# Performance work log

Hardware: AMD Instinct MI355X
Metric: run time of the kernel (lower is better)

The kernel has to match this reference:

```python
import jax, jax.numpy as jnp
import numpy as np


def lstm_cell(x, h, c, Wi, Wh, b):
    # PyTorch LSTMCell gate order: i, f, g, o
    g = x @ Wi.T + h @ Wh.T + b
    i, f, gg, o = jnp.split(g, 4, axis=-1)
    c = jax.nn.sigmoid(f) * c + jax.nn.sigmoid(i) * jnp.tanh(gg)
    h = jax.nn.sigmoid(o) * jnp.tanh(c)
    return h, c


def setup_inputs() -> dict:
    key = jax.random.key(0)
    ks = jax.random.split(key, 32)
    S, B, L, N, T = 20, 16, 30, 6, 20
    H, E, Vs, Vt = 512, 512, 50000, 30000
    w = lambda k, shape: jax.random.normal(k, shape, jnp.float32) * 0.05
    return {
        'articles': jax.random.randint(ks[0], (S, B, L), 0, Vs, jnp.int32),
        'summaries': jax.random.randint(ks[1], (N, B, T), 0, Vt, jnp.int32),
        'emb_src': w(ks[2], (Vs, E)),
        'emb_tgt': w(ks[3], (Vt, E)),
        'we_Wi': w(ks[4], (4 * H, E)), 'we_Wh': w(ks[5], (4 * H, H)), 'we_b': w(ks[6], (4 * H,)),
        'se_Wi': w(ks[7], (4 * H, H)), 'se_Wh': w(ks[8], (4 * H, H)), 'se_b': w(ks[9], (4 * H,)),
        'W_feat': w(ks[10], (H, H)), 'b_feat': w(ks[11], (H,)),
        'wd_Wi': w(ks[12], (4 * H, E)), 'wd_Wh': w(ks[13], (4 * H, H)), 'wd_b': w(ks[14], (4 * H,)),
        'W_vocab': w(ks[15], (Vt, H)), 'b_vocab': w(ks[16], (Vt,)),
        'sd_Wi': w(ks[17], (4 * H, H)), 'sd_Wh': w(ks[18], (4 * H, H)), 'sd_b': w(ks[19], (4 * H,)),
        'attn_Wh': w(ks[20], (H, H)), 'attn_wc': w(ks[21], (H,)), 'attn_v': w(ks[22], (H,)),
        'W_out': w(ks[23], (H, 2 * H)), 'b_out': w(ks[24], (H,)),
    }


def _forward(articles, summaries, emb_src, emb_tgt, we_Wi, we_Wh, we_b,
             se_Wi, se_Wh, se_b, W_feat, b_feat, wd_Wi, wd_Wh, wd_b,
             W_vocab, b_vocab, sd_Wi, sd_Wh, sd_b, attn_Wh, attn_wc, attn_v,
             W_out, b_out):
    S, B, L = articles.shape
    H = we_Wh.shape[1]

    # ---- word encoder: LSTMCell over each sentence, vmapped over S ----
    def encode_sentence(tokens):  # [B, L]
        x = emb_src[tokens]  # [B, L, E]
        z = jnp.zeros((B, H), x.dtype)
        def step(hc, xt):
            h, c = lstm_cell(xt, hc[0], hc[1], we_Wi, we_Wh, we_b)
            return (h, c), None
        (h, _), _ = jax.lax.scan(step, (z, z), jnp.swapaxes(x, 0, 1))
        return h
    word_hx = jax.vmap(encode_sentence)(articles)  # [S, B, H]

    # ---- sentence encoder: LSTM over sentence dim ----
    z = jnp.zeros((B, H), word_hx.dtype)
    def senc_step(hc, x):
        h, c = lstm_cell(x, hc[0], hc[1], se_Wi, se_Wh, se_b)
        return (h, c), h
    (s_hx, s_cx), sent_out = jax.lax.scan(senc_step, (z, z), word_hx)  # sent_out [S,B,H]
    sent_feat = sent_out @ W_feat.T + b_feat  # precomputed attention features

    mask = (articles[:, :, 0:1] > 0).astype(jnp.float32)  # [S, B, 1]
    coverage0 = jnp.zeros_like(mask)

    # ---- hierarchical decoder over summary sentences ----
    def sent_step(carry, sent):  # sent [B, T]
        w_hx, w_cx, s_hx, s_cx, coverage, loss = carry
        seq = sent.T  # [T, B]

        def word_step(wc, ba):
            wh, wcell, l = wc
            wb, wa = ba
            wh, wcell = lstm_cell(emb_tgt[wb], wh, wcell, wd_Wi, wd_Wh, wd_b)
            logits = wh @ W_vocab.T + b_vocab  # [B, V]
            logp = jax.nn.log_softmax(logits, axis=-1)
            nll = -jnp.take_along_axis(logp, wa[:, None], axis=1)[:, 0]
            m = (wa != 0).astype(logits.dtype)  # ignore_index=0
            l = l + jnp.sum(nll * m) / jnp.maximum(jnp.sum(m), 1.0)
            return (wh, wcell, l), None

        (w_hx, w_cx, loss), _ = jax.lax.scan(word_step, (w_hx, w_cx, loss), (seq[:-1], seq[1:]))

        # sentence decoder step with coverage attention over S sentences
        s_h2, s_cx = lstm_cell(w_hx, s_hx, s_cx, sd_Wi, sd_Wh, sd_b)
        e = jnp.einsum('sbh,h->sb', jnp.tanh(sent_feat + s_h2 @ attn_Wh.T + coverage * attn_wc), attn_v)
        e = jnp.where(mask[:, :, 0] > 0, e, -1e9)
        align = jax.nn.softmax(e, axis=0)[:, :, None]  # [S, B, 1]
        context = jnp.sum(align * sent_out, axis=0)  # [B, H]
        final = jnp.tanh(jnp.concatenate([context, s_h2], axis=-1) @ W_out.T + b_out)
        # coverage loss (with pre-update coverage), then accumulate coverage
        loss = loss + jnp.mean(jnp.sum(jnp.minimum(align[:, :, 0], coverage[:, :, 0]), axis=0))
        coverage = coverage + align
        return (final, w_cx, final, s_cx, coverage, loss), None

    init = (s_hx, s_cx, s_hx, s_cx, coverage0, jnp.float32(0.0))
    (_, _, _, _, _, loss), _ = jax.lax.scan(sent_step, init, summaries)
    return loss


def reference(articles, summaries, emb_src, emb_tgt, we_Wi, we_Wh, we_b,
              se_Wi, se_Wh, se_b, W_feat, b_feat, wd_Wi, wd_Wh, wd_b,
              W_vocab, b_vocab, sd_Wi, sd_Wh, sd_b, attn_Wh, attn_wc, attn_v,
              W_out, b_out):
    return _forward(articles, summaries, emb_src, emb_tgt, we_Wi, we_Wh, we_b,
                    se_Wi, se_Wh, se_b, W_feat, b_feat, wd_Wi, wd_Wh, wd_b,
                    W_vocab, b_vocab, sd_Wi, sd_Wh, sd_b, attn_Wh, attn_wc,
                    attn_v, W_out, b_out)
```

## Files before the change

### kernel.cpp

```cpp
#include <hip/hip_runtime.h>
#include <cstdint>
#include <cstddef>

#define H 512
#define SS 20
#define BB 16
#define LL 30
#define NN 6
#define TT 20
#define VT 30000
#define MROWS 1824
#define NSTEPS 114
#define MPAD 1856
#define NT2 120
#define VBLK 232
#define UBLK 16

typedef __attribute__((ext_vector_type(8))) short bf16x8;
typedef __attribute__((ext_vector_type(4))) float f32x4;

__device__ __forceinline__ float sigmoidf_(float x) { return 1.f / (1.f + expf(-x)); }
__device__ __forceinline__ float b2f(ushort u) { return __uint_as_float(((uint32_t)u) << 16); }
__device__ __forceinline__ ushort f2b_rne(float f) {
  uint32_t u = __float_as_uint(f);
  return (ushort)((u + 0x7fffu + ((u >> 16) & 1u)) >> 16);
}

__device__ __forceinline__ void gbar(uint* cnt, uint* gen, uint nblk)
{
  __syncthreads();
  if (threadIdx.x == 0) {
    uint g = __hip_atomic_load(gen, __ATOMIC_RELAXED, __HIP_MEMORY_SCOPE_AGENT);
    uint v = __hip_atomic_fetch_add(cnt, 1u, __ATOMIC_ACQ_REL, __HIP_MEMORY_SCOPE_AGENT);
    if (v == nblk - 1u) {
      __hip_atomic_store(cnt, 0u, __ATOMIC_RELAXED, __HIP_MEMORY_SCOPE_AGENT);
      __hip_atomic_store(gen, g + 1u, __ATOMIC_RELEASE, __HIP_MEMORY_SCOPE_AGENT);
    } else {
      while (__hip_atomic_load(gen, __ATOMIC_ACQUIRE, __HIP_MEMORY_SCOPE_AGENT) == g)
        __builtin_amdgcn_s_sleep(2);
    }
  }
  __syncthreads();
}

struct PrepP {
  const int* articles; const int* summaries;
  const float* emb_src; const float* emb_tgt;
  const float* we_Wi; const float* wd_Wi; const float* we_Wh;
  const float* se_Wi; const float* se_Wh; const float* W_feat;
  const float* wd_Wh; const float* sd_Wi; const float* sd_Wh;
  const float* attn_Wh; const float* W_out;
  ushort* A_we; ushort* A_wd;
  ushort* weWi; ushort* wdWi; ushort* weWh;
  ushort* seWi; ushort* seWh; ushort* wfeat;
  ushort* wdWh; ushort* sdWi; ushort* sdWh;
  ushort* attnWh; ushort* Wout;
};

__device__ __forceinline__ void conv_f2b(const float* __restrict__ src,
                                         ushort* __restrict__ dst, int n4,
                                         int t0, int stride)
{
  for (int i = t0; i < n4; i += stride) {
    float4 v = reinterpret_cast<const float4*>(src)[i];
    ushort4 o;
    o.x = f2b_rne(v.x); o.y = f2b_rne(v.y);
    o.z = f2b_rne(v.z); o.w = f2b_rne(v.w);
    reinterpret_cast<ushort4*>(dst)[i] = o;
  }
}

__global__ __launch_bounds__(256) void prep_kernel(PrepP P)
{
  const int t0 = blockIdx.x * 256 + threadIdx.x;
  const int stride = gridDim.x * 256;
  for (int i = t0; i < SS * BB * LL * H; i += stride) {
    int m = i >> 9, k = i & 511;
    int l = m / (SS * BB), sb = m % (SS * BB);
    int tok = P.articles[sb * LL + l];
    P.A_we[i] = f2b_rne(P.emb_src[(size_t)tok * H + k]);
  }
  for (int i = t0; i < MROWS * H; i += stride) {
    int m = i >> 9, k = i & 511;
    int stp = m >> 4, b = m & 15;
    int n = stp / (TT - 1), t = stp % (TT - 1);
    int tok = P.summaries[(n * BB + b) * TT + t];
    P.A_wd[i] = f2b_rne(P.emb_tgt[(size_t)tok * H + k]);
  }
  const int Q = 4 * H * H / 4;
  conv_f2b(P.we_Wi, P.weWi, Q, t0, stride);
  conv_f2b(P.wd_Wi, P.wdWi, Q, t0, stride);
  conv_f2b(P.we_Wh, P.weWh, Q, t0, stride);
  conv_f2b(P.se_Wi, P.seWi, Q, t0, stride);
  conv_f2b(P.se_Wh, P.seWh, Q, t0, stride);
  conv_f2b(P.wd_Wh, P.wdWh, Q, t0, stride);
  conv_f2b(P.sd_Wi, P.sdWi, Q, t0, stride);
  conv_f2b(P.sd_Wh, P.sdWh, Q, t0, stride);
  conv_f2b(P.W_feat, P.wfeat, H * H / 4, t0, stride);
  conv_f2b(P.attn_Wh, P.attnWh, H * H / 4, t0, stride);
  conv_f2b(P.W_out, P.Wout, H * 2 * H / 4, t0, stride);
}

__global__ __launch_bounds__(512) void proj_mfma_kernel(
    const ushort* __restrict__ A_we, const ushort* __restrict__ weWi,
    const float* __restrict__ we_b, ushort* __restrict__ XiW,
    const ushort* __restrict__ A_wd, const ushort* __restrict__ wdWi,
    const float* __restrict__ wd_b, ushort* __restrict__ XiD)
{
  int bid = blockIdx.x;
  const ushort* A; const ushort* W; const float* bias; ushort* C; int M, mt, nt;
  if (bid < 1200) { A = A_we; W = weWi; bias = we_b; C = XiW; M = 9600; mt = bid >> 3; nt = bid & 7; }
  else { int b2 = bid - 1200; A = A_wd; W = wdWi; bias = wd_b; C = XiD; M = MROWS; mt = b2 >> 3; nt = b2 & 7; }
  const int tid = threadIdx.x, wid = tid >> 6, lane = tid & 63;
  const int wm = wid >> 2, wn = wid & 3;
  const int m0 = mt * 64 + wm * 32, n0 = nt * 256 + wn * 64;
  const int lr = lane & 15, lk = (lane >> 4) << 3;

  f32x4 acc[2][4];
#pragma unroll
  for (int i = 0; i < 2; ++i)
#pragma unroll
    for (int nf = 0; nf < 4; ++nf) acc[i][nf] = (f32x4)0.0f;

  for (int k0 = 0; k0 < H; k0 += 32) {
    bf16x8 a[2], b[4];
#pragma unroll
    for (int i = 0; i < 2; ++i) {
      int m = m0 + i * 16 + lr;
      bf16x8 az = (bf16x8)(short)0;
      if (m < M) az = *reinterpret_cast<const bf16x8*>(A + (size_t)m * H + k0 + lk);
      a[i] = az;
    }
#pragma unroll
    for (int nf = 0; nf < 4; ++nf)
      b[nf] = *reinterpret_cast<const bf16x8*>(W + (size_t)(n0 + nf * 16 + lr) * H + k0 + lk);
#pragma unroll
    for (int i = 0; i < 2; ++i)
#pragma unroll
      for (int nf = 0; nf < 4; ++nf)
        acc[i][nf] = __builtin_amdgcn_mfma_f32_16x16x32_bf16(a[i], b[nf], acc[i][nf], 0, 0, 0);
  }
#pragma unroll
  for (int i = 0; i < 2; ++i)
#pragma unroll
    for (int nf = 0; nf < 4; ++nf) {
      int n = n0 + nf * 16 + lr;
      float bv = bias[n];
#pragma unroll
      for (int jreg = 0; jreg < 4; ++jreg) {
        int row = m0 + i * 16 + (lane >> 4) * 4 + jreg;
        if (row < M) C[(size_t)row * 2048 + n] = f2b_rne(acc[i][nf][jreg] + bv);
      }
    }
}

struct UP {
  const ushort* XiW; const ushort* XiD;
  const ushort* weWh; const ushort* seWi; const ushort* seWh;
  const ushort* wfeat; const ushort* wdWh; const ushort* sdWi;
  const ushort* sdWh; const ushort* attnWh; const ushort* Wout;
  const float* se_b; const float* b_feat; const float* sd_b; const float* b_out;
  const float* attn_wc; const float* attn_v; const int* articles;
  ushort* h0; ushort* h1;
  float* XiS;
  ushort* sh0; ushort* sh1;
  float* sent_out; ushort* sent_out_bf; float* sent_feat;
  ushort* wh_bf; ushort* sdh_bf; ushort* final_bf; ushort* catb;
  float* qb; float* ebuf; float* alignb; float* covb; float* loss;
  uint* bcnt; uint* bgen;
};

__global__ __launch_bounds__(512) void uni_kernel(UP P)
{
  __shared__ f32x4 hred[2][4][64];
  const int tid = threadIdx.x, bid = blockIdx.x;
  const int wid = tid >> 6, lane = tid & 63;
  const int gw = bid * 8 + wid;
  const int lr = lane & 15;
  const int lk = (lane >> 4) << 3;
  const int orow = (lane >> 4) << 2;

  {
    float cst[5][4];
#pragma unroll
    for (int it = 0; it < 5; ++it)
#pragma unroll
      for (int rg = 0; rg < 4; ++rg) cst[it][rg] = 0.f;
    ushort* cur = P.h0;
    ushort* nxt = P.h1;
    const int ug = gw & 31;
    const int unit = ug * 16 + lr;
    const ushort* wb = P.weWh + (size_t)(ug * 16 + lr) * H + lk;
    for (int l = 0; l < LL; ++l) {
#pragma unroll
      for (int it = 0; it < 5; ++it) {
        int item = gw + it * 128;
        int mt = item >> 5;
        f32x4 acc[4];
#pragma unroll
        for (int g = 0; g < 4; ++g) acc[g] = (f32x4)0.0f;
        const ushort* ab = cur + (size_t)(mt * 16 + lr) * H + lk;
#pragma unroll
        for (int k0 = 0; k0 < H; k0 += 32) {
          bf16x8 a = *reinterpret_cast<const bf16x8*>(ab + k0);
#pragma unroll
          for (int g = 0; g < 4; ++g) {
            bf16x8 b = *reinterpret_cast<const bf16x8*>(wb + (size_t)g * H * H + k0);
            acc[g] = __builtin_amdgcn_mfma_f32_16x16x32_bf16(a, b, acc[g], 0, 0, 0);
          }
        }
#pragma unroll
        for (int rg = 0; rg < 4; ++rg) {
          int row = mt * 16 + orow + rg;
          const ushort* xi = P.XiW + (size_t)(l * 320 + row) * 2048 + unit;
          float gi = acc[0][rg] + b2f(xi[0]);
          float gf = acc[1][rg] + b2f(xi[512]);
          float gc = acc[2][rg] + b2f(xi[1024]);
          float go = acc[3][rg] + b2f(xi[1536]);
          float c = sigmoidf_(gf) * cst[it][rg] + sigmoidf_(gi) * tanhf(gc);
          float h = sigmoidf_(go) * tanhf(c);
          cst[it][rg] = c;
          nxt[(size_t)row * H + unit] = f2b_rne(h);
        }
      }
      gbar(P.bcnt, P.bgen, UBLK);
      ushort* t = cur; cur = nxt; nxt = t;
    }
    {
      const ushort* wbs = P.seWi + (size_t)(ug * 16 + lr) * H + lk;
#pragma unroll
      for (int it = 0; it < 5; ++it) {
        int item = gw + it * 128;
        int mt = item >> 5;
        f32x4 acc[4];
#pragma unroll
        for (int g = 0; g < 4; ++g) acc[g] = (f32x4)0.0f;
        const ushort* ab = cur + (size_t)(mt * 16 + lr) * H + lk;
#pragma unroll
        for (int k0 = 0; k0 < H; k0 += 32) {
          bf16x8 a = *reinterpret_cast<const bf16x8*>(ab + k0);
#pragma unroll
          for (int g = 0; g < 4; ++g) {
            bf16x8 b = *reinterpret_cast<const bf16x8*>(wbs + (size_t)g * H * H + k0);
            acc[g] = __builtin_amdgcn_mfma_f32_16x16x32_bf16(a, b, acc[g], 0, 0, 0);
          }
        }
#pragma unroll
        for (int rg = 0; rg < 4; ++rg) {
          int row = mt * 16 + orow + rg;
#pragma unroll
          for (int g = 0; g < 4; ++g)
            P.XiS[(size_t)row * 2048 + g * H + unit] = acc[g][rg] + P.se_b[g * H + unit];
        }
      }
    }
    gbar(P.bcnt, P.bgen, UBLK);
  }

  float cw[4] = {0.f, 0.f, 0.f, 0.f};
  float csd[4] = {0.f, 0.f, 0.f, 0.f};
  {
    float cse[4] = {0.f, 0.f, 0.f, 0.f};
    ushort* cur = P.sh0;
    ushort* nxt = P.sh1;
    const int ug = bid * 2 + wid;
    const int unit = ug * 16 + lr;
    for (int s = 0; s < SS; ++s) {
      if (wid < 2) {
        f32x4 acc[4];
#pragma unroll
        for (int g = 0; g < 4; ++g) acc[g] = (f32x4)0.0f;
        const ushort* ab = cur + (size_t)lr * H + lk;
        const ushort* wb = P.seWh + (size_t)(ug * 16 + lr) * H + lk;
#pragma unroll
        for (int k0 = 0; k0 < H; k0 += 32) {
          bf16x8 a = *reinterpret_cast<const bf16x8*>(ab + k0);
#pragma unroll
          for (int g = 0; g < 4; ++g) {
            bf16x8 b = *reinterpret_cast<const bf16x8*>(wb + (size_t)g * H * H + k0);
            acc[g] = __builtin_amdgcn_mfma_f32_16x16x32_bf16(a, b, acc[g], 0, 0, 0);
          }
        }
#pragma unroll
        for (int rg = 0; rg < 4; ++rg) {
          int row = orow + rg;
          const float* xi = P.XiS + (size_t)(s * 16 + row) * 2048 + unit;
          float gi = acc[0][rg] + xi[0];
          float gf = acc[1][rg] + xi[512];
          float gc = acc[2][rg] + xi[1024];
          float go = acc[3][rg] + xi[1536];
          float c = sigmoidf_(gf) * cse[rg] + sigmoidf_(gi) * tanhf(gc);
          float h = sigmoidf_(go) * tanhf(c);
          cse[rg] = c;
          nxt[(size_t)row * H + unit] = f2b_rne(h);
          P.sent_out[(size_t)(s * 16 + row) * H + unit] = h;
          P.sent_out_bf[(size_t)(s * 16 + row) * H + unit] = f2b_rne(h);
        }
      }
      gbar(P.bcnt, P.bgen, UBLK);
      ushort* t = cur; cur = nxt; nxt = t;
    }
    if (wid < 2) {
      f32x4 v; v[0] = cse[0]; v[1] = cse[1]; v[2] = cse[2]; v[3] = cse[3];
      hred[wid][0][lane] = v;
#pragma unroll
      for (int rg = 0; rg < 4; ++rg) csd[rg] = cse[rg];
    }
    __syncthreads();
    if (wid < 4 && !(wid & 1)) {
      f32x4 v = hred[wid >> 1][0][lane];
      cw[0] = v[0]; cw[1] = v[1]; cw[2] = v[2]; cw[3] = v[3];
    }
    __syncthreads();
  }

  {
    const int ug = gw & 31;
    const int unit = ug * 16 + lr;
    const ushort* wb = P.wfeat + (size_t)(ug * 16 + lr) * H + lk;
#pragma unroll
    for (int it = 0; it < 5; ++it) {
      int item = gw + it * 128;
      int mt = item >> 5;
      f32x4 acc = (f32x4)0.0f;
      const ushort* ab = P.sent_out_bf + (size_t)(mt * 16 + lr) * H + lk;
#pragma unroll
      for (int k0 = 0; k0 < H; k0 += 32) {
        bf16x8 a = *reinterpret_cast<const bf16x8*>(ab + k0);
        bf16x8 b = *reinterpret_cast<const bf16x8*>(wb + k0);
        acc = __builtin_amdgcn_mfma_f32_16x16x32_bf16(a, b, acc, 0, 0, 0);
      }
#pragma unroll
      for (int rg = 0; rg < 4; ++rg) {
        int row = mt * 16 + orow + rg;
        P.sent_feat[(size_t)row * H + unit] = acc[rg] + P.b_feat[unit];
      }
    }
    gbar(P.bcnt, P.bgen, UBLK);
  }

  {
    const int half = wid & 1;
    const int ug2 = bid * 2 + (wid >> 1);
    const int unit2 = ug2 * 16 + lr;
    const int ug = bid * 2 + wid;
    const int unit = ug * 16 + lr;

    for (int n = 0; n < NN; ++n) {
      bf16x8 wreg[4][8];
      if (wid < 4) {
#pragma unroll
        for (int g = 0; g < 4; ++g)
#pragma unroll
          for (int kk = 0; kk < 8; ++kk)
            wreg[g][kk] = *reinterpret_cast<const bf16x8*>(
                P.wdWh + (size_t)g * H * H + (size_t)(ug2 * 16 + lr) * H +
                half * 256 + kk * 32 + lk);
      }
      for (int t = 0; t < TT - 1; ++t) {
        int stp = n * (TT - 1) + t;
        f32x4 acc[4];
        if (wid < 4) {
          const ushort* A = (t == 0)
              ? ((n == 0) ? P.sh0 : P.final_bf)
              : P.wh_bf + (size_t)(stp - 1) * 16 * H;
#pragma unroll
          for (int g = 0; g < 4; ++g) acc[g] = (f32x4)0.0f;
          const ushort* ab = A + (size_t)lr * H + half * 256 + lk;
#pragma unroll
          for (int kk = 0; kk < 8; ++kk) {
            bf16x8 a = *reinterpret_cast<const bf16x8*>(ab + kk * 32);
#pragma unroll
            for (int g = 0; g < 4; ++g)
              acc[g] = __builtin_amdgcn_mfma_f32_16x16x32_bf16(a, wreg[g][kk], acc[g], 0, 0, 0);
          }
          if (half) {
#pragma unroll
            for (int g = 0; g < 4; ++g) hred[wid >> 1][g][lane] = acc[g];
          }
        }
        __syncthreads();
        if (wid < 4 && !half) {
#pragma unroll
          for (int g = 0; g < 4; ++g) {
            f32x4 o = hred[wid >> 1][g][lane];
            acc[g] += o;
          }
#pragma unroll
          for (int rg = 0; rg < 4; ++rg) {
            int row = orow + rg;
            const ushort* xi = P.XiD + (size_t)(stp * 16 + row) * 2048 + unit2;
            float gi = acc[0][rg] + b2f(xi[0]);
            float gf = acc[1][rg] + b2f(xi[512]);
            float gc = acc[2][rg] + b2f(xi[1024]);
            float go = acc[3][rg] + b2f(xi[1536]);
            float c = sigmoidf_(gf) * cw[rg] + sigmoidf_(gi) * tanhf(gc);
            float h = sigmoidf_(go) * tanhf(c);
            cw[rg] = c;
            P.wh_bf[(size_t)(stp * 16 + row) * H + unit2] = f2b_rne(h);
          }
        }
        gbar(P.bcnt, P.bgen, UBLK);
      }
      if (wid < 2) {
        f32x4 acc[4];
#pragma unroll
        for (int g = 0; g < 4; ++g) acc[g] = (f32x4)0.0f;
        const ushort* A1 = P.wh_bf + (size_t)(n * (TT - 1) + TT - 2) * 16 * H;
        const ushort* A2 = (n == 0) ? P.sh0 : P.final_bf;
        const ushort* ab1 = A1 + (size_t)lr * H + lk;
        const ushort* wb1 = P.sdWi + (size_t)(ug * 16 + lr) * H + lk;
#pragma unroll
        for (int k0 = 0; k0 < H; k0 += 32) {
          bf16x8 a = *reinterpret_cast<const bf16x8*>(ab1 + k0);
#pragma unroll
          for (int g = 0; g < 4; ++g) {
            bf16x8 b = *reinterpret_cast<const bf16x8*>(wb1 + (size_t)g * H * H + k0);
            acc[g] = __builtin_amdgcn_mfma_f32_16x16x32_bf16(a, b, acc[g], 0, 0, 0);
          }
        }
        const ushort* ab2 = A2 + (size_t)lr * H + lk;
        const ushort* wb2 = P.sdWh + (size_t)(ug * 16 + lr) * H + lk;
#pragma unroll
        for (int k0 = 0; k0 < H; k0 += 32) {
          bf16x8 a = *reinterpret_cast<const bf16x8*>(ab2 + k0);
#pragma unroll
          for (int g = 0; g < 4; ++g) {
            bf16x8 b = *reinterpret_cast<const bf16x8*>(wb2 + (size_t)g * H * H + k0);
            acc[g] = __builtin_amdgcn_mfma_f32_16x16x32_bf16(a, b, acc[g], 0, 0, 0);
          }
        }
#pragma unroll
        for (int rg = 0; rg < 4; ++rg) {
          int row = orow + rg;
          float gi = acc[0][rg] + P.sd_b[0 * H + unit];
          float gf = acc[1][rg] + P.sd_b[1 * H + unit];
          float gc = acc[2][rg] + P.sd_b[2 * H + unit];
          float go = acc[3][rg] + P.sd_b[3 * H + unit];
          float c = sigmoidf_(gf) * csd[rg] + sigmoidf_(gi) * tanhf(gc);
          float h = sigmoidf_(go) * tanhf(c);
          csd[rg] = c;
          P.sdh_bf[(size_t)row * H + unit] = f2b_rne(h);
        }
      }
      gbar(P.bcnt, P.bgen, UBLK);
      if (wid < 2) {
        f32x4 acc = (f32x4)0.0f;
        const ushort* ab = P.sdh_bf + (size_t)lr * H + lk;
        const ushort* wb = P.attnWh + (size_t)(ug * 16 + lr) * H + lk;
#pragma unroll
        for (int k0 = 0; k0 < H; k0 += 32) {
          bf16x8 a = *reinterpret_cast<const bf16x8*>(ab + k0);
          bf16x8 b = *reinterpret_cast<const bf16x8*>(wb + k0);
          acc = __builtin_amdgcn_mfma_f32_16x16x32_bf16(a, b, acc, 0, 0, 0);
        }
#pragma unroll
        for (int rg = 0; rg < 4; ++rg)
          P.qb[(size_t)(orow + rg) * H + unit] = acc[rg];
      }
      gbar(P.bcnt, P.bgen, UBLK);
      for (int sb = gw; sb < 320; sb += 128) {
        int b = sb & 15;
        float cov = P.covb[sb];
        float sum = 0.f;
        for (int h2 = lane; h2 < H; h2 += 64)
          sum += tanhf(P.sent_feat[(size_t)sb * H + h2] + P.qb[b * H + h2] +
                       cov * P.attn_wc[h2]) * P.attn_v[h2];
#pragma unroll
        for (int d = 1; d < 64; d <<= 1) sum += __shfl_xor(sum, d);
        if (lane == 0)
          P.ebuf[sb] = (P.articles[sb * LL] > 0) ? sum : -1e9f;
      }
      gbar(P.bcnt, P.bgen, UBLK);
      if (wid == 0) {
        int b = bid;
        float ev = (lane < SS) ? P.ebuf[lane * 16 + b] : -3.0e38f;
        float mx = ev;
#pragma unroll
        for (int d = 1; d < 64; d <<= 1) mx = fmaxf(mx, __shfl_xor(mx, d));
        float ex = (lane < SS) ? expf(ev - mx) : 0.f;
        float s = ex;
#pragma unroll
        for (int d = 1; d < 64; d <<= 1) s += __shfl_xor(s, d);
        float al = ex / s;
        float cl = 0.f;
        if (lane < SS) {
          int sb = lane * 16 + b;
          float cov = P.covb[sb];
          cl = fminf(al, cov);
          P.covb[sb] = cov + al;
          P.alignb[sb] = al;
        }
#pragma unroll
        for (int d = 1; d < 64; d <<= 1) cl += __shfl_xor(cl, d);
        if (lane == 0) atomicAdd(P.loss, cl * (1.f / BB));
      }
      gbar(P.bcnt, P.bgen, UBLK);
      {
        int idx = bid * 512 + tid;
        int b = idx >> 9, h2 = idx & 511;
        float s = 0.f;
#pragma unroll
        for (int ss2 = 0; ss2 < SS; ++ss2)
          s += P.alignb[ss2 * 16 + b] * P.sent_out[(size_t)(ss2 * 16 + b) * H + h2];
        P.catb[b * 1024 + h2] = f2b_rne(s);
        P.catb[b * 1024 + 512 + h2] = P.sdh_bf[(size_t)b * H + h2];
      }
      gbar(P.bcnt, P.bgen, UBLK);
      if (wid < 2) {
        f32x4 acc = (f32x4)0.0f;
        const ushort* ab = P.catb + (size_t)lr * 1024 + lk;
        const ushort* wb = P.Wout + (size_t)(ug * 16 + lr) * 1024 + lk;
#pragma unroll
        for (int k0 = 0; k0 < 1024; k0 += 32) {
          bf16x8 a = *reinterpret_cast<const bf16x8*>(ab + k0);
          bf16x8 b = *reinterpret_cast<const bf16x8*>(wb + k0);
          acc = __builtin_amdgcn_mfma_f32_16x16x32_bf16(a, b, acc, 0, 0, 0);
        }
#pragma unroll
        for (int rg = 0; rg < 4; ++rg) {
          int row = orow + rg;
          float v = tanhf(acc[rg] + P.b_out[unit]);
          P.final_bf[(size_t)row * H + unit] = f2b_rne(v);
        }
      }
      gbar(P.bcnt, P.bgen, UBLK);
    }
  }
}

__global__ __launch_bounds__(512) void vocab_kernel(
    const ushort* __restrict__ A, const float* __restrict__ Wf,
    ushort* __restrict__ Wbf, const float* __restrict__ bias,
    float* __restrict__ partials, uint* bcnt, uint* bgen)
{
  {
    int t0 = blockIdx.x * 512 + threadIdx.x;
    const int n4 = VT * H / 4;
    for (int i = t0; i < n4; i += VBLK * 512) {
      float4 v = reinterpret_cast<const float4*>(Wf)[i];
      ushort4 o;
      o.x = f2b_rne(v.x); o.y = f2b_rne(v.y);
      o.z = f2b_rne(v.z); o.w = f2b_rne(v.w);
      reinterpret_cast<ushort4*>(Wbf)[i] = o;
    }
  }
  gbar(bcnt, bgen, VBLK);

  __shared__ float red[4][64][2];
  const int bid = blockIdx.x;
  const int chunk = bid & 7, mt = bid >> 3;
  const int tid = threadIdx.x;
  const int wid = tid >> 6, lane = tid & 63;
  const int wm = wid >> 2, wn = wid & 3;
  const int m0 = mt * 64 + wm * 32;
  const int lr = lane & 15;
  const int lk = (lane >> 4) << 3;

  bf16x8 areg[2][16];
#pragma unroll
  for (int i = 0; i < 2; ++i)
#pragma unroll
    for (int kk = 0; kk < 16; ++kk)
      areg[i][kk] = *reinterpret_cast<const bf16x8*>(
          A + (size_t)(m0 + i * 16 + lr) * H + kk * 32 + lk);

  for (int nt2 = 0; nt2 < 15; ++nt2) {
    const int n0 = chunk * 3840 + nt2 * 256 + wn * 64;
    f32x4 acc[2][4];
#pragma unroll
    for (int i = 0; i < 2; ++i)
#pragma unroll
      for (int nf = 0; nf < 4; ++nf) acc[i][nf] = (f32x4)0.0f;

#pragma unroll 4
    for (int kk = 0; kk < 16; ++kk) {
      bf16x8 b[4];
#pragma unroll
      for (int nf = 0; nf < 4; ++nf) {
        int n = n0 + nf * 16 + lr;
        bf16x8 bz = (bf16x8)(short)0;
        if (n < VT) bz = *reinterpret_cast<const bf16x8*>(Wbf + (size_t)n * H + kk * 32 + lk);
        b[nf] = bz;
      }
#pragma unroll
      for (int i = 0; i < 2; ++i)
#pragma unroll
        for (int nf = 0; nf < 4; ++nf)
          acc[i][nf] = __builtin_amdgcn_mfma_f32_16x16x32_bf16(areg[i][kk], b[nf], acc[i][nf], 0, 0, 0);
    }

    float bc[4];
    int val[4];
#pragma unroll
    for (int nf = 0; nf < 4; ++nf) {
      int n = n0 + nf * 16 + lr;
      val[nf] = (n < VT);
      bc[nf] = val[nf] ? bias[n] : 0.f;
    }
#pragma unroll
    for (int i = 0; i < 2; ++i) {
#pragma unroll
      for (int jreg = 0; jreg < 4; ++jreg) {
        float lg[4];
        float mx = -3.0e38f;
#pragma unroll
        for (int nf = 0; nf < 4; ++nf) {
          lg[nf] = val[nf] ? (acc[i][nf][jreg] + bc[nf]) : -3.0e38f;
          mx = fmaxf(mx, lg[nf]);
        }
#pragma unroll
        for (int d = 1; d < 16; d <<= 1) mx = fmaxf(mx, __shfl_xor(mx, d));
        float s = 0.f;
#pragma unroll
        for (int nf = 0; nf < 4; ++nf) s += val[nf] ? expf(lg[nf] - mx) : 0.f;
#pragma unroll
        for (int d = 1; d < 16; d <<= 1) s += __shfl_xor(s, d);
        if (lr == 0) {
          int rloc = wm * 32 + i * 16 + (lane >> 4) * 4 + jreg;
          red[wn][rloc][0] = mx;
          red[wn][rloc][1] = s;
        }
      }
    }
    __syncthreads();
    if (tid < 64) {
      int r2 = tid;
      float M = -3.0e38f;
#pragma unroll
      for (int w = 0; w < 4; ++w) M = fmaxf(M, red[w][r2][0]);
      float S = 0.f;
#pragma unroll
      for (int w = 0; w < 4; ++w) S += red[w][r2][1] * expf(red[w][r2][0] - M);
      size_t p = ((size_t)(mt * 64 + r2) * NT2 + chunk * 15 + nt2) * 2;
      partials[p] = M;
      partials[p + 1] = S;
    }
    __syncthreads();
  }
}

__global__ void tlog_kernel(const ushort* __restrict__ wh_bf,
                            const ushort* __restrict__ Wv_bf,
                            const float* __restrict__ bv,
                            const int* __restrict__ summaries,
                            float* __restrict__ tlog)
{
  int row = blockIdx.x;
  int lane = threadIdx.x;
  int b = row & 15, stp = row >> 4;
  int n = stp / (TT - 1), t = stp % (TT - 1);
  int tgt = summaries[(n * BB + b) * TT + t + 1];
  float s = 0.f;
  for (int k = lane; k < H; k += 64)
    s += b2f(wh_bf[(size_t)row * H + k]) * b2f(Wv_bf[(size_t)tgt * H + k]);
#pragma unroll
  for (int d = 1; d < 64; d <<= 1) s += __shfl_xor(s, d);
  if (lane == 0) tlog[row] = s + bv[tgt];
}

__global__ __launch_bounds__(256) void nll_kernel(
    const float* __restrict__ partials, const float* __restrict__ tlog,
    const int* __restrict__ summaries, float* __restrict__ loss)
{
  int stp = blockIdx.x;
  int tid = threadIdx.x;
  int rr = tid >> 4, ch = tid & 15;
  int row = stp * 16 + rr;
  const float* pr = partials + (size_t)row * NT2 * 2;
  float mx = -3.0e38f;
  for (int t2 = ch; t2 < NT2; t2 += 16) mx = fmaxf(mx, pr[t2 * 2]);
#pragma unroll
  for (int d = 1; d < 16; d <<= 1) mx = fmaxf(mx, __shfl_xor(mx, d));
  float s = 0.f;
  for (int t2 = ch; t2 < NT2; t2 += 16) s += pr[t2 * 2 + 1] * expf(pr[t2 * 2] - mx);
#pragma unroll
  for (int d = 1; d < 16; d <<= 1) s += __shfl_xor(s, d);
  __shared__ float sh_n[16], sh_m[16];
  if (ch == 0) {
    float lse = mx + logf(s);
    float nll = lse - tlog[row];
    int b = row & 15;
    int n = stp / (TT - 1), t = stp % (TT - 1);
    int wa = summaries[(n * BB + b) * TT + t + 1];
    sh_n[rr] = (wa != 0) ? nll : 0.f;
    sh_m[rr] = (wa != 0) ? 1.f : 0.f;
  }
  __syncthreads();
  if (tid == 0) {
    float sn = 0.f, sm = 0.f;
    for (int r2 = 0; r2 < 16; ++r2) { sn += sh_n[r2]; sm += sh_m[r2]; }
    atomicAdd(loss, sn / fmaxf(sm, 1.f));
  }
}

extern "C" void kernel_launch(void* const* d_in, const int* in_sizes, int n_in,
                              void* d_out, int out_size, void* d_ws, size_t ws_size,
                              hipStream_t stream)
{
  (void)in_sizes; (void)n_in; (void)out_size; (void)ws_size;
  const int*   articles  = (const int*)d_in[0];
  const int*   summaries = (const int*)d_in[1];
  const float* emb_src   = (const float*)d_in[2];
  const float* emb_tgt   = (const float*)d_in[3];
  const float* we_Wi = (const float*)d_in[4];
  const float* we_Wh = (const float*)d_in[5];
  const float* we_b  = (const float*)d_in[6];
  const float* se_Wi = (const float*)d_in[7];
  const float* se_Wh = (const float*)d_in[8];
  const float* se_b  = (const float*)d_in[9];
  const float* W_feat = (const float*)d_in[10];
  const float* b_feat = (const float*)d_in[11];
  const float* wd_Wi = (const float*)d_in[12];
  const float* wd_Wh = (const float*)d_in[13];
  const float* wd_b  = (const float*)d_in[14];
  const float* W_vocab = (const float*)d_in[15];
  const float* b_vocab = (const float*)d_in[16];
  const float* sd_Wi = (const float*)d_in[17];
  const float* sd_Wh = (const float*)d_in[18];
  const float* sd_b  = (const float*)d_in[19];
  const float* attn_Wh = (const float*)d_in[20];
  const float* attn_wc = (const float*)d_in[21];
  const float* attn_v  = (const float*)d_in[22];
  const float* W_out = (const float*)d_in[23];
  const float* b_out = (const float*)d_in[24];

  char* wsb = (char*)d_ws;
  size_t off = 0;
  auto alloc = [&](size_t bytes) -> char* {
    char* p = wsb + off;
    off += (bytes + 255) & ~(size_t)255;
    return p;
  };

  char* regA = alloc(9830400);
  ushort* A_we     = (ushort*)regA;
  ushort* wh_bf    = (ushort*)regA;
  float*  partials = (float*)(regA + 1900544);
  float*  tlogb    = (float*)(regA + 3682304);

  ushort* A_wd = (ushort*)alloc((size_t)MROWS * H * 2);

  char* regW = alloc((size_t)9600 * 2048 * 2);
  ushort* XiW   = (ushort*)regW;
  ushort* Wv_bf = (ushort*)regW;

  ushort* XiD = (ushort*)alloc((size_t)MROWS * 2048 * 2);

  ushort* weWi  = (ushort*)alloc(4 * H * H * 2);
  ushort* wdWi  = (ushort*)alloc(4 * H * H * 2);
  ushort* weWh  = (ushort*)alloc(4 * H * H * 2);
  ushort* seWi  = (ushort*)alloc(4 * H * H * 2);
  ushort* seWh  = (ushort*)alloc(4 * H * H * 2);
  ushort* wdWh  = (ushort*)alloc(4 * H * H * 2);
  ushort* sdWi  = (ushort*)alloc(4 * H * H * 2);
  ushort* sdWh  = (ushort*)alloc(4 * H * H * 2);
  ushort* wfeat = (ushort*)alloc(H * H * 2);
  ushort* attnWh= (ushort*)alloc(H * H * 2);
  ushort* Wout  = (ushort*)alloc(H * 2 * H * 2);

  float*  XiS = (float*)alloc((size_t)320 * 2048 * 4);
  ushort* h0  = (ushort*)alloc(320 * H * 2);
  ushort* h1  = (ushort*)alloc(320 * H * 2);
  ushort* sh0 = (ushort*)alloc(16 * H * 2);
  ushort* sh1 = (ushort*)alloc(16 * H * 2);
  float*  sent_out    = (float*)alloc(320 * H * 4);
  ushort* sent_out_bf = (ushort*)alloc(320 * H * 2);
  float*  sent_feat   = (float*)alloc(320 * H * 4);
  ushort* sdh_bf   = (ushort*)alloc(16 * H * 2);
  ushort* final_bf = (ushort*)alloc(16 * H * 2);
  ushort* catb     = (ushort*)alloc(16 * 1024 * 2);
  float*  qb       = (float*)alloc(16 * H * 4);
  float*  ebuf   = (float*)alloc(1280);
  float*  alignb = (float*)alloc(1280);
  float*  covb   = (float*)alloc(1280);
  uint*   bar    = (uint*)alloc(256);

  float* loss = (float*)d_out;
  hipMemsetAsync(loss, 0, 4, stream);
  hipMemsetAsync(covb, 0, 1280, stream);
  hipMemsetAsync(h0, 0, 320 * H * 2, stream);
  hipMemsetAsync(sh0, 0, 16 * H * 2, stream);
  hipMemsetAsync(bar, 0, 256, stream);

  {
    PrepP P = {articles, summaries, emb_src, emb_tgt,
               we_Wi, wd_Wi, we_Wh, se_Wi, se_Wh, W_feat,
               wd_Wh, sd_Wi, sd_Wh, attn_Wh, W_out,
               A_we, A_wd, weWi, wdWi, weWh, seWi, seWh, wfeat,
               wdWh, sdWi, sdWh, attnWh, Wout};
    prep_kernel<<<2048, 256, 0, stream>>>(P);
  }

  proj_mfma_kernel<<<1432, 512, 0, stream>>>(A_we, weWi, we_b, XiW,
                                             A_wd, wdWi, wd_b, XiD);

  hipMemsetAsync((char*)wh_bf + (size_t)MROWS * H * 2, 0,
                 (size_t)(MPAD - MROWS) * H * 2, stream);

  {
    UP P;
    P.XiW = XiW; P.XiD = XiD;
    P.weWh = weWh; P.seWi = seWi; P.seWh = seWh; P.wfeat = wfeat;
    P.wdWh = wdWh; P.sdWi = sdWi; P.sdWh = sdWh; P.attnWh = attnWh; P.Wout = Wout;
    P.se_b = se_b; P.b_feat = b_feat; P.sd_b = sd_b; P.b_out = b_out;
    P.attn_wc = attn_wc; P.attn_v = attn_v; P.articles = articles;
    P.h0 = h0; P.h1 = h1; P.XiS = XiS; P.sh0 = sh0; P.sh1 = sh1;
    P.sent_out = sent_out; P.sent_out_bf = sent_out_bf; P.sent_feat = sent_feat;
    P.wh_bf = wh_bf; P.sdh_bf = sdh_bf; P.final_bf = final_bf; P.catb = catb;
    P.qb = qb; P.ebuf = ebuf; P.alignb = alignb; P.covb = covb; P.loss = loss;
    P.bcnt = bar; P.bgen = bar + 1;
    uni_kernel<<<UBLK, 512, 0, stream>>>(P);
  }

  vocab_kernel<<<VBLK, 512, 0, stream>>>(wh_bf, W_vocab, Wv_bf, b_vocab,
                                         partials, bar + 2, bar + 3);
  tlog_kernel<<<MROWS, 64, 0, stream>>>(wh_bf, Wv_bf, b_vocab, summaries, tlogb);
  nll_kernel<<<NSTEPS, 256, 0, stream>>>(partials, tlogb, summaries, loss);
}
```

Measured before the change: 5.198 ms.

## Fuse vocab projection into recurrent kernel with flag-based overlap and flag barriers

Merges the serial recurrent kernel and the vocab-logsumexp kernel into one launch of 248 blocks. The 232 vocab blocks convert W_vocab to bf16 while the 16 recurrent blocks run, then each starts its GEMM as soon as the decoder rows it needs are published through a progress flag. The counter/generation grid barrier is replaced by per-block phase flags polled in parallel, and one barrier in the decoder loop becomes a local __syncthreads. This relies on all 248 blocks being co-resident and on the memory ordering of the flag protocol, and the vocab blocks may compete with the latency-bound recurrence for bandwidth.

```diff
diff --git a/kernel.cpp b/kernel.cpp
--- a/kernel.cpp
+++ b/kernel.cpp
@@ -13,8 +13,11 @@
 #define NSTEPS 114
 #define MPAD 1856
 #define NT2 120
-#define VBLK 232
 #define UBLK 16
+#define NV 232
+#define MEGA 248
+
+#define SCOPE_AGENT __HIP_MEMORY_SCOPE_AGENT
 
 typedef __attribute__((ext_vector_type(8))) short bf16x8;
 typedef __attribute__((ext_vector_type(4))) float f32x4;
@@ -26,20 +29,27 @@
   return (ushort)((u + 0x7fffu + ((u >> 16) & 1u)) >> 16);
 }
 
-__device__ __forceinline__ void gbar(uint* cnt, uint* gen, uint nblk)
+__device__ __forceinline__ void ast_u32(uint* p, uint v) {
+  __hip_atomic_store(p, v, __ATOMIC_RELAXED, SCOPE_AGENT);
+}
+__device__ __forceinline__ uint ald_u32(const uint* p) {
+  return __hip_atomic_load(p, __ATOMIC_RELAXED, SCOPE_AGENT);
+}
+
+__device__ __forceinline__ void sbar(uint* flags, int slot, int nblk, uint phase)
 {
   __syncthreads();
   if (threadIdx.x == 0) {
-    uint g = __hip_atomic_load(gen, __ATOMIC_RELAXED, __HIP_MEMORY_SCOPE_AGENT);
-    uint v = __hip_atomic_fetch_add(cnt, 1u, __ATOMIC_ACQ_REL, __HIP_MEMORY_SCOPE_AGENT);
-    if (v == nblk - 1u) {
-      __hip_atomic_store(cnt, 0u, __ATOMIC_RELAXED, __HIP_MEMORY_SCOPE_AGENT);
-      __hip_atomic_store(gen, g + 1u, __ATOMIC_RELEASE, __HIP_MEMORY_SCOPE_AGENT);
-    } else {
-      while (__hip_atomic_load(gen, __ATOMIC_ACQUIRE, __HIP_MEMORY_SCOPE_AGENT) == g)
-        __builtin_amdgcn_s_sleep(2);
-    }
-  }
+    __builtin_amdgcn_fence(__ATOMIC_RELEASE, "agent");
+    ast_u32(&flags[slot * 16], phase);
+  }
+  if ((int)threadIdx.x < nblk) {
+    while (ald_u32(&flags[threadIdx.x * 16]) < phase)
+      __builtin_amdgcn_s_sleep(1);
+  }
+  __syncthreads();
+  if (threadIdx.x == 0)
+    __builtin_amdgcn_fence(__ATOMIC_ACQUIRE, "agent");
   __syncthreads();
 }
 
@@ -154,7 +164,7 @@
     }
 }
 
-struct UP {
+struct MP {
   const ushort* XiW; const ushort* XiD;
   const ushort* weWh; const ushort* seWi; const ushort* seWh;
   const ushort* wfeat; const ushort* wdWh; const ushort* sdWi;
@@ -167,18 +177,140 @@
   float* sent_out; ushort* sent_out_bf; float* sent_feat;
   ushort* wh_bf; ushort* sdh_bf; ushort* final_bf; ushort* catb;
   float* qb; float* ebuf; float* alignb; float* covb; float* loss;
-  uint* bcnt; uint* bgen;
+  uint* sflags;
+  uint* vbflags;
+  uint* vflag;
+  const float* Wv; ushort* Wv_bf; const float* bv; float* partials;
 };
 
-__global__ __launch_bounds__(512) void uni_kernel(UP P)
+__global__ __launch_bounds__(512) void mega_kernel(MP P)
 {
-  __shared__ f32x4 hred[2][4][64];
   const int tid = threadIdx.x, bid = blockIdx.x;
   const int wid = tid >> 6, lane = tid & 63;
-  const int gw = bid * 8 + wid;
   const int lr = lane & 15;
   const int lk = (lane >> 4) << 3;
   const int orow = (lane >> 4) << 2;
+
+  if (bid >= UBLK) {
+    const int v = bid - UBLK;
+    const int mt = v >> 3, chunk = v & 7;
+    __shared__ float red[4][64][2];
+
+    if (tid == 0) {
+      while (ald_u32(P.vflag) < 1u) __builtin_amdgcn_s_sleep(16);
+    }
+    __syncthreads();
+    {
+      const int n4 = VT * H / 4;
+      for (int i = v * 512 + tid; i < n4; i += NV * 512) {
+        float4 w = reinterpret_cast<const float4*>(P.Wv)[i];
+        ushort4 o;
+        o.x = f2b_rne(w.x); o.y = f2b_rne(w.y);
+        o.z = f2b_rne(w.z); o.w = f2b_rne(w.w);
+        reinterpret_cast<ushort4*>(P.Wv_bf)[i] = o;
+      }
+    }
+    sbar(P.vbflags, v, NV, 1u);
+
+    {
+      int lastStep = mt * 4 + 3; if (lastStep > 113) lastStep = 113;
+      uint want = 2u + (uint)(lastStep / 19);
+      if (tid == 0) {
+        while (ald_u32(P.vflag) < want) __builtin_amdgcn_s_sleep(16);
+        __builtin_amdgcn_fence(__ATOMIC_ACQUIRE, "agent");
+      }
+      __syncthreads();
+    }
+
+    const int wm = wid >> 2, wn = wid & 3;
+    const int m0 = mt * 64 + wm * 32;
+    bf16x8 areg[2][16];
+#pragma unroll
+    for (int i = 0; i < 2; ++i)
+#pragma unroll
+      for (int kk = 0; kk < 16; ++kk)
+        areg[i][kk] = *reinterpret_cast<const bf16x8*>(
+            P.wh_bf + (size_t)(m0 + i * 16 + lr) * H + kk * 32 + lk);
+
+    for (int nt2 = 0; nt2 < 15; ++nt2) {
+      const int n0 = chunk * 3840 + nt2 * 256 + wn * 64;
+      f32x4 acc[2][4];
+#pragma unroll
+      for (int i = 0; i < 2; ++i)
+#pragma unroll
+        for (int nf = 0; nf < 4; ++nf) acc[i][nf] = (f32x4)0.0f;
+
+#pragma unroll 4
+      for (int kk = 0; kk < 16; ++kk) {
+        bf16x8 b[4];
+#pragma unroll
+        for (int nf = 0; nf < 4; ++nf) {
+          int n = n0 + nf * 16 + lr;
+          bf16x8 bz = (bf16x8)(short)0;
+          if (n < VT) bz = *reinterpret_cast<const bf16x8*>(P.Wv_bf + (size_t)n * H + kk * 32 + lk);
+          b[nf] = bz;
+        }
+#pragma unroll
+        for (int i = 0; i < 2; ++i)
+#pragma unroll
+          for (int nf = 0; nf < 4; ++nf)
+            acc[i][nf] = __builtin_amdgcn_mfma_f32_16x16x32_bf16(areg[i][kk], b[nf], acc[i][nf], 0, 0, 0);
+      }
+
+      float bc[4];
+      int val[4];
+#pragma unroll
+      for (int nf = 0; nf < 4; ++nf) {
+        int n = n0 + nf * 16 + lr;
+        val[nf] = (n < VT);
+        bc[nf] = val[nf] ? P.bv[n] : 0.f;
+      }
+#pragma unroll
+      for (int i = 0; i < 2; ++i) {
+#pragma unroll
+        for (int jreg = 0; jreg < 4; ++jreg) {
+          float lg[4];
+          float mx = -3.0e38f;
+#pragma unroll
+          for (int nf = 0; nf < 4; ++nf) {
+            lg[nf] = val[nf] ? (acc[i][nf][jreg] + bc[nf]) : -3.0e38f;
+            mx = fmaxf(mx, lg[nf]);
+          }
+#pragma unroll
+          for (int d = 1; d < 16; d <<= 1) mx = fmaxf(mx, __shfl_xor(mx, d));
+          float s = 0.f;
+#pragma unroll
+          for (int nf = 0; nf < 4; ++nf) s += val[nf] ? expf(lg[nf] - mx) : 0.f;
+#pragma unroll
+          for (int d = 1; d < 16; d <<= 1) s += __shfl_xor(s, d);
+          if (lr == 0) {
+            int rloc = wm * 32 + i * 16 + (lane >> 4) * 4 + jreg;
+            red[wn][rloc][0] = mx;
+            red[wn][rloc][1] = s;
+          }
+        }
+      }
+      __syncthreads();
+      if (tid < 64) {
+        int r2 = tid;
+        float M = -3.0e38f;
+#pragma unroll
+        for (int w = 0; w < 4; ++w) M = fmaxf(M, red[w][r2][0]);
+        float S = 0.f;
+#pragma unroll
+        for (int w = 0; w < 4; ++w) S += red[w][r2][1] * expf(red[w][r2][0] - M);
+        size_t p = ((size_t)(mt * 64 + r2) * NT2 + chunk * 15 + nt2) * 2;
+        P.partials[p] = M;
+        P.partials[p + 1] = S;
+      }
+      __syncthreads();
+    }
+    return;
+  }
+
+  __shared__ f32x4 hred[2][4][64];
+  const int gw = bid * 8 + wid;
+  uint ph = 0;
 
   {
     float cst[5][4];
@@ -194,8 +326,7 @@
     for (int l = 0; l < LL; ++l) {
 #pragma unroll
       for (int it = 0; it < 5; ++it) {
-        int item = gw + it * 128;
-        int mt = item >> 5;
+        int mt = (gw + it * 128) >> 5;
         f32x4 acc[4];
 #pragma unroll
         for (int g = 0; g < 4; ++g) acc[g] = (f32x4)0.0f;
@@ -223,15 +354,14 @@
           nxt[(size_t)row * H + unit] = f2b_rne(h);
         }
       }
-      gbar(P.bcnt, P.bgen, UBLK);
+      sbar(P.sflags, bid, UBLK, ++ph);
       ushort* t = cur; cur = nxt; nxt = t;
     }
     {
       const ushort* wbs = P.seWi + (size_t)(ug * 16 + lr) * H + lk;
 #pragma unroll
       for (int it = 0; it < 5; ++it) {
-        int item = gw + it * 128;
-        int mt = item >> 5;
+        int mt = (gw + it * 128) >> 5;
         f32x4 acc[4];
 #pragma unroll
         for (int g = 0; g < 4; ++g) acc[g] = (f32x4)0.0f;
@@ -254,7 +384,9 @@
         }
       }
     }
-    gbar(P.bcnt, P.bgen, UBLK);
+    sbar(P.sflags, bid, UBLK, ++ph);
+    if (bid == 0 && tid == 0)
+      __hip_atomic_store(P.vflag, 1u, __ATOMIC_RELEASE, SCOPE_AGENT);
   }
 
   float cw[4] = {0.f, 0.f, 0.f, 0.f};
@@ -297,7 +429,7 @@
           P.sent_out_bf[(size_t)(s * 16 + row) * H + unit] = f2b_rne(h);
         }
       }
-      gbar(P.bcnt, P.bgen, UBLK);
+      sbar(P.sflags, bid, UBLK, ++ph);
       ushort* t = cur; cur = nxt; nxt = t;
     }
     if (wid < 2) {
@@ -320,8 +452,7 @@
     const ushort* wb = P.wfeat + (size_t)(ug * 16 + lr) * H + lk;
 #pragma unroll
     for (int it = 0; it < 5; ++it) {
-      int item = gw + it * 128;
-      int mt = item >> 5;
+      int mt = (gw + it * 128) >> 5;
       f32x4 acc = (f32x4)0.0f;
       const ushort* ab = P.sent_out_bf + (size_t)(mt * 16 + lr) * H + lk;
 #pragma unroll
@@ -336,7 +467,7 @@
         P.sent_feat[(size_t)row * H + unit] = acc[rg] + P.b_feat[unit];
       }
     }
-    gbar(P.bcnt, P.bgen, UBLK);
+    sbar(P.sflags, bid, UBLK, ++ph);
   }
 
   {
@@ -382,10 +513,7 @@
         __syncthreads();
         if (wid < 4 && !half) {
 #pragma unroll
-          for (int g = 0; g < 4; ++g) {
-            f32x4 o = hred[wid >> 1][g][lane];
-            acc[g] += o;
-          }
+          for (int g = 0; g < 4; ++g) acc[g] += hred[wid >> 1][g][lane];
 #pragma unroll
           for (int rg = 0; rg < 4; ++rg) {
             int row = orow + rg;
@@ -400,8 +528,10 @@
             P.wh_bf[(size_t)(stp * 16 + row) * H + unit2] = f2b_rne(h);
           }
         }
-        gbar(P.bcnt, P.bgen, UBLK);
-      }
+        sbar(P.sflags, bid, UBLK, ++ph);
+      }
+      if (bid == 0 && tid == 0)
+        __hip_atomic_store(P.vflag, 2u + (uint)n, __ATOMIC_RELEASE, SCOPE_AGENT);
       if (wid < 2) {
         f32x4 acc[4];
 #pragma unroll
@@ -443,7 +573,7 @@
           P.sdh_bf[(size_t)row * H + unit] = f2b_rne(h);
         }
       }
-      gbar(P.bcnt, P.bgen, UBLK);
+      sbar(P.sflags, bid, UBLK, ++ph);
       if (wid < 2) {
         f32x4 acc = (f32x4)0.0f;
         const ushort* ab = P.sdh_bf + (size_t)lr * H + lk;
@@ -458,7 +588,7 @@
         for (int rg = 0; rg < 4; ++rg)
           P.qb[(size_t)(orow + rg) * H + unit] = acc[rg];
       }
-      gbar(P.bcnt, P.bgen, UBLK);
+      sbar(P.sflags, bid, UBLK, ++ph);
       for (int sb = gw; sb < 320; sb += 128) {
         int b = sb & 15;
         float cov = P.covb[sb];
@@ -471,7 +601,7 @@
         if (lane == 0)
           P.ebuf[sb] = (P.articles[sb * LL] > 0) ? sum : -1e9f;
       }
-      gbar(P.bcnt, P.bgen, UBLK);
+      sbar(P.sflags, bid, UBLK, ++ph);
       if (wid == 0) {
         int b = bid;
         float ev = (lane < SS) ? P.ebuf[lane * 16 + b] : -3.0e38f;
@@ -495,10 +625,9 @@
         for (int d = 1; d < 64; d <<= 1) cl += __shfl_xor(cl, d);
         if (lane == 0) atomicAdd(P.loss, cl * (1.f / BB));
       }
-      gbar(P.bcnt, P.bgen, UBLK);
+      __syncthreads();
       {
-        int idx = bid * 512 + tid;
-        int b = idx >> 9, h2 = idx & 511;
+        int b = bid, h2 = tid;
         float s = 0.f;
 #pragma unroll
         for (int ss2 = 0; ss2 < SS; ++ss2)
@@ -506,7 +635,7 @@
         P.catb[b * 1024 + h2] = f2b_rne(s);
         P.catb[b * 1024 + 512 + h2] = P.sdh_bf[(size_t)b * H + h2];
       }
-      gbar(P.bcnt, P.bgen, UBLK);
+      sbar(P.sflags, bid, UBLK, ++ph);
       if (wid < 2) {
         f32x4 acc = (f32x4)0.0f;
         const ushort* ab = P.catb + (size_t)lr * 1024 + lk;
@@ -524,119 +653,10 @@
           P.final_bf[(size_t)row * H + unit] = f2b_rne(v);
         }
       }
-      gbar(P.bcnt, P.bgen, UBLK);
-    }
-  }
-}
-
-__global__ __launch_bounds__(512) void vocab_kernel(
-    const ushort* __restrict__ A, const float* __restrict__ Wf,
-    ushort* __restrict__ Wbf, const float* __restrict__ bias,
-    float* __restrict__ partials, uint* bcnt, uint* bgen)
-{
-  {
-    int t0 = blockIdx.x * 512 + threadIdx.x;
-    const int n4 = VT * H / 4;
-    for (int i = t0; i < n4; i += VBLK * 512) {
-      float4 v = reinterpret_cast<const float4*>(Wf)[i];
-      ushort4 o;
-      o.x = f2b_rne(v.x); o.y = f2b_rne(v.y);
-      o.z = f2b_rne(v.z); o.w = f2b_rne(v.w);
-      reinterpret_cast<ushort4*>(Wbf)[i] = o;
-    }
-  }
-  gbar(bcnt, bgen, VBLK);
-
-  __shared__ float red[4][64][2];
-  const int bid = blockIdx.x;
-  const int chunk = bid & 7, mt = bid >> 3;
-  const int tid = threadIdx.x;
-  const int wid = tid >> 6, lane = tid & 63;
-  const int wm = wid >> 2, wn = wid & 3;
-  const int m0 = mt * 64 + wm * 32;
-  const int lr = lane & 15;
-  const int lk = (lane >> 4) << 3;
-
-  bf16x8 areg[2][16];
-#pragma unroll
-  for (int i = 0; i < 2; ++i)
-#pragma unroll
-    for (int kk = 0; kk < 16; ++kk)
-      areg[i][kk] = *reinterpret_cast<const bf16x8*>(
-          A + (size_t)(m0 + i * 16 + lr) * H + kk * 32 + lk);
-
-  for (int nt2 = 0; nt2 < 15; ++nt2) {
-    const int n0 = chunk * 3840 + nt2 * 256 + wn * 64;
-    f32x4 acc[2][4];
-#pragma unroll
-    for (int i = 0; i < 2; ++i)
-#pragma unroll
-      for (int nf = 0; nf < 4; ++nf) acc[i][nf] = (f32x4)0.0f;
-
-#pragma unroll 4
-    for (int kk = 0; kk < 16; ++kk) {
-      bf16x8 b[4];
-#pragma unroll
-      for (int nf = 0; nf < 4; ++nf) {
-        int n = n0 + nf * 16 + lr;
-        bf16x8 bz = (bf16x8)(short)0;
-        if (n < VT) bz = *reinterpret_cast<const bf16x8*>(Wbf + (size_t)n * H + kk * 32 + lk);
-        b[nf] = bz;
-      }
-#pragma unroll
-      for (int i = 0; i < 2; ++i)
-#pragma unroll
-        for (int nf = 0; nf < 4; ++nf)
-          acc[i][nf] = __builtin_amdgcn_mfma_f32_16x16x32_bf16(areg[i][kk], b[nf], acc[i][nf], 0, 0, 0);
-    }
-
-    float bc[4];
-    int val[4];
-#pragma unroll
-    for (int nf = 0; nf < 4; ++nf) {
-      int n = n0 + nf * 16 + lr;
-      val[nf] = (n < VT);
-      bc[nf] = val[nf] ? bias[n] : 0.f;
-    }
-#pragma unroll
-    for (int i = 0; i < 2; ++i) {
-#pragma unroll
-      for (int jreg = 0; jreg < 4; ++jreg) {
-        float lg[4];
-        float mx = -3.0e38f;
-#pragma unroll
-        for (int nf = 0; nf < 4; ++nf) {
-          lg[nf] = val[nf] ? (acc[i][nf][jreg] + bc[nf]) : -3.0e38f;
-          mx = fmaxf(mx, lg[nf]);
-        }
-#pragma unroll
-        for (int d = 1; d < 16; d <<= 1) mx = fmaxf(mx, __shfl_xor(mx, d));
-        float s = 0.f;
-#pragma unroll
-        for (int nf = 0; nf < 4; ++nf) s += val[nf] ? expf(lg[nf] - mx) : 0.f;
-#pragma unroll
-        for (int d = 1; d < 16; d <<= 1) s += __shfl_xor(s, d);
-        if (lr == 0) {
-          int rloc = wm * 32 + i * 16 + (lane >> 4) * 4 + jreg;
-          red[wn][rloc][0] = mx;
-          red[wn][rloc][1] = s;
-        }
-      }
-    }
-    __syncthreads();
-    if (tid < 64) {
-      int r2 = tid;
-      float M = -3.0e38f;
-#pragma unroll
-      for (int w = 0; w < 4; ++w) M = fmaxf(M, red[w][r2][0]);
-      float S = 0.f;
-#pragma unroll
-      for (int w = 0; w < 4; ++w) S += red[w][r2][1] * expf(red[w][r2][0] - M);
-      size_t p = ((size_t)(mt * 64 + r2) * NT2 + chunk * 15 + nt2) * 2;
-      partials[p] = M;
-      partials[p + 1] = S;
-    }
-    __syncthreads();
+      sbar(P.sflags, bid, UBLK, ++ph);
+    }
+    if (bid == 0 && tid == 0)
+      __hip_atomic_store(P.vflag, 7u, __ATOMIC_RELEASE, SCOPE_AGENT);
   }
 }
 
@@ -774,14 +794,18 @@
   float*  ebuf   = (float*)alloc(1280);
   float*  alignb = (float*)alloc(1280);
   float*  covb   = (float*)alloc(1280);
-  uint*   bar    = (uint*)alloc(256);
+  uint*   sflags  = (uint*)alloc(UBLK * 16 * 4);
+  uint*   vbflags = (uint*)alloc(NV * 16 * 4);
+  uint*   vflag   = (uint*)alloc(256);
 
   float* loss = (float*)d_out;
   hipMemsetAsync(loss, 0, 4, stream);
   hipMemsetAsync(covb, 0, 1280, stream);
   hipMemsetAsync(h0, 0, 320 * H * 2, stream);
   hipMemsetAsync(sh0, 0, 16 * H * 2, stream);
-  hipMemsetAsync(bar, 0, 256, stream);
+  hipMemsetAsync(sflags, 0, UBLK * 16 * 4, stream);
+  hipMemsetAsync(vbflags, 0, NV * 16 * 4, stream);
+  hipMemsetAsync(vflag, 0, 256, stream);
 
   {
     PrepP P = {articles, summaries, emb_src, emb_tgt,
@@ -799,7 +823,7 @@
                  (size_t)(MPAD - MROWS) * H * 2, stream);
 
   {
-    UP P;
+    MP P;
     P.XiW = XiW; P.XiD = XiD;
     P.weWh = weWh; P.seWi = seWi; P.seWh = seWh; P.wfeat = wfeat;
     P.wdWh = wdWh; P.sdWi = sdWi; P.sdWh = sdWh; P.attnWh = attnWh; P.Wout = Wout;
@@ -809,12 +833,11 @@
     P.sent_out = sent_out; P.sent_out_bf = sent_out_bf; P.sent_feat = sent_feat;
     P.wh_bf = wh_bf; P.sdh_bf = sdh_bf; P.final_bf = final_bf; P.catb = catb;
     P.qb = qb; P.ebuf = ebuf; P.alignb = alignb; P.covb = covb; P.loss = loss;
-    P.bcnt = bar; P.bgen = bar + 1;
-    uni_kernel<<<UBLK, 512, 0, stream>>>(P);
-  }
-
-  vocab_kernel<<<VBLK, 512, 0, stream>>>(wh_bf, W_vocab, Wv_bf, b_vocab,
-                                         partials, bar + 2, bar + 3);
+    P.sflags = sflags; P.vbflags = vbflags; P.vflag = vflag;
+    P.Wv = W_vocab; P.Wv_bf = Wv_bf; P.bv = b_vocab; P.partials = partials;
+    mega_kernel<<<MEGA, 512, 0, stream>>>(P);
+  }
+
   tlog_kernel<<<MROWS, 64, 0, stream>>>(wh_bf, Wv_bf, b_vocab, summaries, tlogb);
   nll_kernel<<<NSTEPS, 256, 0, stream>>>(partials, tlogb, summaries, loss);
 }
```

New measurement: 5.032 ms. 1.03x faster.
